# Kernel tuning notes

Hardware: AMD Instinct MI355X
Metric: run time of the kernel (lower is better)

The kernel has to match this reference:

```python
import jax, jax.numpy as jnp
import numpy as np

B, IC, OC, K, H, W = 8, 512, 512, 3, 32, 32
GAIN, LRMUL = 1.0, 1.0
# compute_runtime_coef: fan_in = prod(weight_shape[:-1])
RC_CONV = GAIN / np.sqrt(K * K * IC) * LRMUL   # conv weight [K,K,IC,OC]
RC_DENSE = GAIN / np.sqrt(IC) * LRMUL          # dense weight [IC, IC]


def setup_inputs() -> dict:
    key = jax.random.key(0)
    ks = jax.random.split(key, 4)
    x = jax.random.normal(ks[0], (B, IC, H, W), dtype=jnp.float32)
    w = jax.random.normal(ks[1], (B, IC), dtype=jnp.float32)
    # init_std = 1/lrmul = 1.0 for both weights; bias init zeros
    conv_w = jax.random.normal(ks[2], (K, K, IC, OC), dtype=jnp.float32)
    dense_w = jax.random.normal(ks[3], (IC, IC), dtype=jnp.float32)
    dense_b = jnp.zeros((IC,), dtype=jnp.float32)
    return {"x": x, "w": w, "conv_w": conv_w, "dense_w": dense_w, "dense_b": dense_b}


def reference(x, w, conv_w, dense_w, dense_b):
    b, ic, h, wd = x.shape
    # modulation: style = Dense(w) + bias + 1
    style = w @ (RC_DENSE * dense_w) + LRMUL * dense_b + 1.0        # [B, IC]
    wt = (RC_CONV * conv_w)[None] * style[:, None, None, :, None]   # [B,K,K,IC,OC]
    # demodulation: rsqrt of sum of squares over (kh, kw, ic)
    d = jax.lax.rsqrt(jnp.sum(jnp.square(wt), axis=(1, 2, 3)) + 1e-8)  # [B, OC]
    wt = wt * d[:, None, None, None, :]
    # grouped conv with groups = batch: weight -> OIHW [B*OC, IC, K, K]
    w_g = jnp.transpose(wt, (0, 4, 3, 1, 2)).reshape(b * OC, ic, K, K)
    xg = x.reshape(1, b * ic, h, wd)
    y = jax.lax.conv_general_dilated(
        xg, w_g, window_strides=(1, 1), padding="SAME",
        dimension_numbers=("NCHW", "OIHW", "NCHW"), feature_group_count=b)
    return y.reshape(b, OC, h, wd)
```

## Files before the change

### kernel.cpp

```cpp
#include <hip/hip_runtime.h>
#include <stdint.h>


#define B_   8
#define IC_  512
#define OC_  512

static constexpr float RC_DENSE = 0.04419417382415922f;
static constexpr float RC_CONV  = 0.014731391274719739f;

typedef _Float16 half8    __attribute__((ext_vector_type(8)));
typedef float    floatx16 __attribute__((ext_vector_type(16)));

__device__ __forceinline__ void g2l(const void* g, void* l) {
  __builtin_amdgcn_global_load_lds(
      (const __attribute__((address_space(1))) void*)g,
      (__attribute__((address_space(3))) void*)l, 16, 0, 0);
}

__global__ __launch_bounds__(256) void style_kernel(
    const float* __restrict__ wv, const float* __restrict__ dw,
    const float* __restrict__ db, float* __restrict__ sm,
    float* __restrict__ sm2) {
  const int b = blockIdx.y;
  const int i = blockIdx.x * 64 + (threadIdx.x & 63);
  const int jg = threadIdx.x >> 6;
  __shared__ float red[4][64];
  float p = 0.f;
  for (int j = jg * 128; j < jg * 128 + 128; ++j)
    p += wv[b * IC_ + j] * dw[(size_t)j * IC_ + i];
  red[jg][threadIdx.x & 63] = p;
  __syncthreads();
  if (threadIdx.x < 64) {
    float s = red[0][threadIdx.x] + red[1][threadIdx.x] +
              red[2][threadIdx.x] + red[3][threadIdx.x];
    s = s * RC_DENSE + db[i] + 1.0f;
    float v = s * RC_CONV;
    sm[b * IC_ + i] = v;
    sm2[b * IC_ + i] = v * v;
  }
}

__global__ __launch_bounds__(256) void prep_kernel(
    const float* __restrict__ cw, const float* __restrict__ x,
    const float* __restrict__ sm, const float* __restrict__ sm2,
    _Float16* __restrict__ Wtf, float* __restrict__ dpart,
    _Float16* __restrict__ xsp) {
  __shared__ __align__(16) char smem[33280];
  const int bid = blockIdx.x;
  const int tid = threadIdx.x;
  if (bid < 256) {
    _Float16* LA = (_Float16*)smem;
    float* redall = (float*)(smem + 18432);
    const int by2 = bid >> 4, icb = bid & 15;
    const int by = by2 >> 1, h2 = by2 & 1;
    const int oc0 = by * 64 + h2 * 32, ic0 = icb * 32;
    const int ocl = tid & 31, g = tid >> 5;
    float sq4[4] = {};
    for (int m = 0; m < 36; ++m) {
      int r = m * 8 + g;
      int t = r >> 5, icl = r & 31;
      float v = cw[(size_t)(t * IC_ + ic0 + icl) * OC_ + oc0 + ocl];
      sq4[m & 3] += v * v;
      LA[m * 256 + ocl * 8 + g] = (_Float16)v;
    }
    for (int b = 0; b < 8; ++b) {
      float p = 0.f;
      for (int s = 0; s < 4; ++s)
        p += sm2[b * IC_ + ic0 + g + 8 * s] * sq4[s];
      redall[(b * 8 + g) * 32 + ocl] = p;
    }
    __syncthreads();
    _Float16* dst = Wtf + (size_t)(by * 16 + icb) * 18432;
    for (int it = 0; it < 5; ++it) {
      int c = it * 256 + tid;
      if (c < 1152) {
        int m = c >> 5, o2 = c & 31;
        *(half8*)(dst + (size_t)(m * 64 + h2 * 32 + o2) * 8) =
            *(const half8*)&LA[m * 256 + o2 * 8];
      }
    }
    const int bb = tid >> 5, o3 = tid & 31;
    float s = 0.f;
    for (int g2 = 0; g2 < 8; ++g2) s += redall[(bb * 8 + g2) * 32 + o3];
    dpart[(size_t)icb * 4096 + bb * OC_ + oc0 + o3] = s;
  } else {
    _Float16* Xt = (_Float16*)smem;
    const int rb = bid - 256;
    const int b = rb >> 5, h = rb & 31;
    for (int k = 0; k < 16; ++k) {
      int idx = k * 256 + tid;
      int ic = idx >> 3, wc = (idx & 7) * 4;
      float4 v = *(const float4*)&x[((size_t)(b * IC_ + ic) * 32 + h) * 32 + wc];
      float s = sm[b * IC_ + ic];
      Xt[(wc + 0) * 520 + ic] = (_Float16)(v.x * s);
      Xt[(wc + 1) * 520 + ic] = (_Float16)(v.y * s);
      Xt[(wc + 2) * 520 + ic] = (_Float16)(v.z * s);
      Xt[(wc + 3) * 520 + ic] = (_Float16)(v.w * s);
    }
    __syncthreads();
    _Float16* xb = xsp + (size_t)b * 16 * 36992;
    const int r = h + 1;
    half8 z = {};
    for (int it = 0; it < 9; ++it) {
      int c = it * 256 + tid;
      if (c < 2176) {
        int icb = c / 136, rem = c - 136 * icb, kkq = rem / 34, C = rem - 34 * kkq;
        half8 val = z;
        if (C != 0 && C != 33)
          val = *(const half8*)&Xt[(C - 1) * 520 + icb * 32 + kkq * 8];
        *(half8*)&xb[(size_t)icb * 36992 + (size_t)r * 1088 + kkq * 272 + C * 8] = val;
      }
    }
    if (h == 0 || h == 31) {
      const int rz = (h == 0) ? 0 : 33;
      for (int it = 0; it < 9; ++it) {
        int c = it * 256 + tid;
        if (c < 2176) {
          int icb = c / 136, rem = c - 136 * icb, kkq = rem / 34, C = rem - 34 * kkq;
          *(half8*)&xb[(size_t)icb * 36992 + (size_t)rz * 1088 + kkq * 272 + C * 8] = z;
        }
      }
    }
  }
}

__global__ __launch_bounds__(256) void conv_kernel(
    const _Float16* __restrict__ Wtf,
    const _Float16* __restrict__ xsp,
    const float* __restrict__ dpart,
    float* __restrict__ out) {
  const int by = blockIdx.x, bx = blockIdx.y, b = blockIdx.z;
  const int tid = threadIdx.x, lane = tid & 63, w = tid >> 6;
  const int wm = w & 1, wn = w >> 1;
  const int n = lane & 31, kq = lane >> 5;
  const int h0 = bx * 4;

  __shared__ _Float16 Xb[2][6528];
  __shared__ float redd[4][64];
  __shared__ float dvl[64];

  const _Float16* gX = xsp + (size_t)b * 16 * 36992 + (size_t)h0 * 1088;
  const _Float16* gA = Wtf + (size_t)(by * 16) * 18432;
  const int aoff = kq * 512 + (wm * 32 + n) * 8;

  for (int i = 0; i < 4; ++i) {
    int c = i * 256 + tid;
    if (c < 816) g2l(gX + (size_t)c * 8, &Xb[0][c * 8]);
  }
  half8 a[9][2], an[9][2];
#pragma unroll
  for (int t = 0; t < 9; ++t)
#pragma unroll
    for (int kk = 0; kk < 2; ++kk)
      a[t][kk] = *(const half8*)(gA + aoff + (t * 2 + kk) * 1024);

  floatx16 acc[2] = {};
  for (int icb = 0; icb < 16; ++icb) {
    const int cur = icb & 1;
    __syncthreads();
    if (icb < 15) {
      const _Float16* gA1 = gA + (size_t)(icb + 1) * 18432 + aoff;
#pragma unroll
      for (int t = 0; t < 9; ++t)
#pragma unroll
        for (int kk = 0; kk < 2; ++kk)
          an[t][kk] = *(const half8*)(gA1 + (t * 2 + kk) * 1024);
      const _Float16* gX1 = gX + (size_t)(icb + 1) * 36992;
      for (int i = 0; i < 4; ++i) {
        int c = i * 256 + tid;
        if (c < 816) g2l(gX1 + (size_t)c * 8, &Xb[cur ^ 1][c * 8]);
      }
    }
    const _Float16* Xp = &Xb[cur][0] + (wn * 2) * 1088 + kq * 272 + n * 8;
#pragma unroll
    for (int s = 0; s < 4; ++s) {
#pragma unroll
      for (int kw = 0; kw < 3; ++kw) {
#pragma unroll
        for (int kk = 0; kk < 2; ++kk) {
          half8 xv = *(const half8*)(Xp + s * 1088 + kk * 544 + kw * 8);
#pragma unroll
          for (int kh = 0; kh < 3; ++kh) {
            int j = s - kh;
            if (j >= 0 && j < 2)
              acc[j] = __builtin_amdgcn_mfma_f32_32x32x16_f16(
                  a[kh * 3 + kw][kk], xv, acc[j], 0, 0, 0);
          }
        }
      }
    }
#pragma unroll
    for (int t = 0; t < 9; ++t) { a[t][0] = an[t][0]; a[t][1] = an[t][1]; }
  }

  __syncthreads();
  {
    const int oc_l = tid & 63, ig = tid >> 6;
    float s = 0.f;
    for (int k = 0; k < 4; ++k)
      s += dpart[(size_t)(ig * 4 + k) * 4096 + b * OC_ + by * 64 + oc_l];
    redd[ig][oc_l] = s;
  }
  __syncthreads();
  if (tid < 64)
    dvl[tid] = rsqrtf(redd[0][tid] + redd[1][tid] + redd[2][tid] +
                      redd[3][tid] + 1e-8f);
  __syncthreads();
  const int oc0 = by * 64 + wm * 32;
  const int r0 = h0 + wn * 2;
#pragma unroll
  for (int rg = 0; rg < 16; ++rg) {
    const int row = (rg & 3) + 8 * (rg >> 2) + 4 * kq;
    const float dv = dvl[wm * 32 + row];
    float* op = out + ((size_t)b * OC_ + oc0 + row) * 1024 + r0 * 32 + n;
    op[0]  = acc[0][rg] * dv;
    op[32] = acc[1][rg] * dv;
  }
}

extern "C" void kernel_launch(void* const* d_in, const int* in_sizes, int n_in,
                              void* d_out, int out_size, void* d_ws, size_t ws_size,
                              hipStream_t stream) {
  const float* x       = (const float*)d_in[0];
  const float* w       = (const float*)d_in[1];
  const float* conv_w  = (const float*)d_in[2];
  const float* dense_w = (const float*)d_in[3];
  const float* dense_b = (const float*)d_in[4];
  float* out = (float*)d_out;

  char* ws = (char*)d_ws;
  float*    sm    = (float*)ws;
  float*    sm2   = (float*)(ws + (16 << 10));
  float*    dpart = (float*)(ws + (32 << 10));
  _Float16* Wtf   = (_Float16*)(ws + (288 << 10));
  _Float16* xsp   = (_Float16*)(ws + (288 << 10) + 4718592);

  style_kernel<<<dim3(8, B_), 256, 0, stream>>>(w, dense_w, dense_b, sm, sm2);
  prep_kernel<<<512, 256, 0, stream>>>(conv_w, x, sm, sm2, Wtf, dpart, xsp);
  conv_kernel<<<dim3(8, 8, B_), 256, 0, stream>>>(Wtf, xsp, dpart, out);
}
```

Baseline: 130.1 us.

## Restructure conv into per-wave independent tiles and atomic demod accumulation

The conv kernel now uses 128-thread blocks in which each wave owns a private LDS double buffer for its input rows. Waits on its own loads use explicit vmcnt counts, so no block-level barriers are needed. Weight fragments are loaded from global at the start of each icb iteration instead of being prefetched into registers, and the grid doubles to 16x8x8 with 32 output channels per block. Demodulation partial sums are atomically accumulated in prep into a buffer zeroed by the style kernel, which removes the 16-way reduction and shared-memory epilogue. This risks exposing the latency of the A loads and duplicates X loads across output-channel groups.

Result: slower. 136.2 us (+4.6%).

```diff
diff --git a/kernel.cpp b/kernel.cpp
--- a/kernel.cpp
+++ b/kernel.cpp
@@ -21,7 +21,7 @@
 __global__ __launch_bounds__(256) void style_kernel(
     const float* __restrict__ wv, const float* __restrict__ dw,
     const float* __restrict__ db, float* __restrict__ sm,
-    float* __restrict__ sm2) {
+    float* __restrict__ sm2, float* __restrict__ dacc) {
   const int b = blockIdx.y;
   const int i = blockIdx.x * 64 + (threadIdx.x & 63);
   const int jg = threadIdx.x >> 6;
@@ -38,13 +38,14 @@
     float v = s * RC_CONV;
     sm[b * IC_ + i] = v;
     sm2[b * IC_ + i] = v * v;
+    dacc[b * IC_ + i] = 0.f;
   }
 }
 
 __global__ __launch_bounds__(256) void prep_kernel(
     const float* __restrict__ cw, const float* __restrict__ x,
     const float* __restrict__ sm, const float* __restrict__ sm2,
-    _Float16* __restrict__ Wtf, float* __restrict__ dpart,
+    _Float16* __restrict__ Wtf, float* __restrict__ dacc,
     _Float16* __restrict__ xsp) {
   __shared__ __align__(16) char smem[33280];
   const int bid = blockIdx.x;
@@ -83,7 +84,7 @@
     const int bb = tid >> 5, o3 = tid & 31;
     float s = 0.f;
     for (int g2 = 0; g2 < 8; ++g2) s += redall[(bb * 8 + g2) * 32 + o3];
-    dpart[(size_t)icb * 4096 + bb * OC_ + oc0 + o3] = s;
+    atomicAdd(&dacc[bb * OC_ + oc0 + o3], s);
   } else {
     _Float16* Xt = (_Float16*)smem;
     const int rb = bid - 256;
@@ -125,54 +126,49 @@
   }
 }
 
-__global__ __launch_bounds__(256) void conv_kernel(
+__global__ __launch_bounds__(128, 2) void conv_kernel(
     const _Float16* __restrict__ Wtf,
     const _Float16* __restrict__ xsp,
-    const float* __restrict__ dpart,
+    const float* __restrict__ dacc,
     float* __restrict__ out) {
-  const int by = blockIdx.x, bx = blockIdx.y, b = blockIdx.z;
-  const int tid = threadIdx.x, lane = tid & 63, w = tid >> 6;
-  const int wm = w & 1, wn = w >> 1;
+  const int og = blockIdx.x;
+  const int rq = blockIdx.y, b = blockIdx.z;
+  const int w = threadIdx.x >> 6, lane = threadIdx.x & 63;
+  const int rp = rq * 2 + w;
   const int n = lane & 31, kq = lane >> 5;
-  const int h0 = bx * 4;
-
-  __shared__ _Float16 Xb[2][6528];
-  __shared__ float redd[4][64];
-  __shared__ float dvl[64];
-
-  const _Float16* gX = xsp + (size_t)b * 16 * 36992 + (size_t)h0 * 1088;
-  const _Float16* gA = Wtf + (size_t)(by * 16) * 18432;
-  const int aoff = kq * 512 + (wm * 32 + n) * 8;
-
-  for (int i = 0; i < 4; ++i) {
-    int c = i * 256 + tid;
-    if (c < 816) g2l(gX + (size_t)c * 8, &Xb[0][c * 8]);
-  }
-  half8 a[9][2], an[9][2];
-#pragma unroll
-  for (int t = 0; t < 9; ++t)
-#pragma unroll
-    for (int kk = 0; kk < 2; ++kk)
-      a[t][kk] = *(const half8*)(gA + aoff + (t * 2 + kk) * 1024);
+  const int R = rp * 2;
+
+  __shared__ __align__(16) _Float16 Xw[2][2][4608];
+
+  const _Float16* gX = xsp + (size_t)b * 16 * 36992 + (size_t)R * 1088;
+  const _Float16* gA = Wtf + (size_t)((og >> 1) * 16) * 18432
+                       + kq * 512 + ((og & 1) * 32 + n) * 8;
+
+  for (int i = 0; i < 9; ++i)
+    g2l(gX + (size_t)(i * 64 + lane) * 8, &Xw[w][0][(i * 64 + lane) * 8]);
+  asm volatile("" ::: "memory");
 
   floatx16 acc[2] = {};
   for (int icb = 0; icb < 16; ++icb) {
     const int cur = icb & 1;
-    __syncthreads();
+    const _Float16* gAi = gA + (size_t)icb * 18432;
+    half8 a[9][2];
+#pragma unroll
+    for (int t = 0; t < 9; ++t)
+#pragma unroll
+      for (int kk = 0; kk < 2; ++kk)
+        a[t][kk] = *(const half8*)(gAi + (t * 2 + kk) * 1024);
     if (icb < 15) {
-      const _Float16* gA1 = gA + (size_t)(icb + 1) * 18432 + aoff;
-#pragma unroll
-      for (int t = 0; t < 9; ++t)
-#pragma unroll
-        for (int kk = 0; kk < 2; ++kk)
-          an[t][kk] = *(const half8*)(gA1 + (t * 2 + kk) * 1024);
       const _Float16* gX1 = gX + (size_t)(icb + 1) * 36992;
-      for (int i = 0; i < 4; ++i) {
-        int c = i * 256 + tid;
-        if (c < 816) g2l(gX1 + (size_t)c * 8, &Xb[cur ^ 1][c * 8]);
-      }
-    }
-    const _Float16* Xp = &Xb[cur][0] + (wn * 2) * 1088 + kq * 272 + n * 8;
+#pragma unroll
+      for (int i = 0; i < 9; ++i)
+        g2l(gX1 + (size_t)(i * 64 + lane) * 8,
+            &Xw[w][cur ^ 1][(i * 64 + lane) * 8]);
+      asm volatile("s_waitcnt vmcnt(27)" ::: "memory");
+    } else {
+      asm volatile("s_waitcnt vmcnt(18)" ::: "memory");
+    }
+    const _Float16* Xp = &Xw[w][cur][0] + kq * 272 + n * 8;
 #pragma unroll
     for (int s = 0; s < 4; ++s) {
 #pragma unroll
@@ -190,30 +186,14 @@
         }
       }
     }
-#pragma unroll
-    for (int t = 0; t < 9; ++t) { a[t][0] = an[t][0]; a[t][1] = an[t][1]; }
-  }
-
-  __syncthreads();
-  {
-    const int oc_l = tid & 63, ig = tid >> 6;
-    float s = 0.f;
-    for (int k = 0; k < 4; ++k)
-      s += dpart[(size_t)(ig * 4 + k) * 4096 + b * OC_ + by * 64 + oc_l];
-    redd[ig][oc_l] = s;
-  }
-  __syncthreads();
-  if (tid < 64)
-    dvl[tid] = rsqrtf(redd[0][tid] + redd[1][tid] + redd[2][tid] +
-                      redd[3][tid] + 1e-8f);
-  __syncthreads();
-  const int oc0 = by * 64 + wm * 32;
-  const int r0 = h0 + wn * 2;
+  }
+
+  const int oc0 = og * 32;
 #pragma unroll
   for (int rg = 0; rg < 16; ++rg) {
     const int row = (rg & 3) + 8 * (rg >> 2) + 4 * kq;
-    const float dv = dvl[wm * 32 + row];
-    float* op = out + ((size_t)b * OC_ + oc0 + row) * 1024 + r0 * 32 + n;
+    const float dv = rsqrtf(dacc[b * OC_ + oc0 + row] + 1e-8f);
+    float* op = out + ((size_t)b * OC_ + oc0 + row) * 1024 + R * 32 + n;
     op[0]  = acc[0][rg] * dv;
     op[32] = acc[1][rg] * dv;
   }
@@ -230,13 +210,13 @@
   float* out = (float*)d_out;
 
   char* ws = (char*)d_ws;
-  float*    sm    = (float*)ws;
-  float*    sm2   = (float*)(ws + (16 << 10));
-  float*    dpart = (float*)(ws + (32 << 10));
-  _Float16* Wtf   = (_Float16*)(ws + (288 << 10));
-  _Float16* xsp   = (_Float16*)(ws + (288 << 10) + 4718592);
-
-  style_kernel<<<dim3(8, B_), 256, 0, stream>>>(w, dense_w, dense_b, sm, sm2);
-  prep_kernel<<<512, 256, 0, stream>>>(conv_w, x, sm, sm2, Wtf, dpart, xsp);
-  conv_kernel<<<dim3(8, 8, B_), 256, 0, stream>>>(Wtf, xsp, dpart, out);
-}
+  float*    sm   = (float*)ws;
+  float*    sm2  = (float*)(ws + (16 << 10));
+  float*    dacc = (float*)(ws + (32 << 10));
+  _Float16* Wtf  = (_Float16*)(ws + (48 << 10));
+  _Float16* xsp  = (_Float16*)(ws + (48 << 10) + 4718592);
+
+  style_kernel<<<dim3(8, B_), 256, 0, stream>>>(w, dense_w, dense_b, sm, sm2, dacc);
+  prep_kernel<<<512, 256, 0, stream>>>(conv_w, x, sm, sm2, Wtf, dacc, xsp);
+  conv_kernel<<<dim3(16, 8, B_), 128, 0, stream>>>(Wtf, xsp, dacc, out);
+}
```
